# Kernel tuning notes

Measured on AMD Instinct MI355X. Metric: run time of the kernel, lower is better.

Reference implementation:

```python
import jax, jax.numpy as jnp
import numpy as np
import math

H, W, K = 512, 512, 256
EPS = 1e-6


def _make_grid(H, W):
    # Faithful to make_coord_grid: grid[a, b] = (xs[a], ys[b]) after the
    # torch meshgrid('xy') + permute(1,0,2) dance. With H == W this is (H, W, 2).
    xs = jnp.linspace(-1.0, 1.0, W)
    ys = jnp.linspace(-1.0, 1.0, H)
    X, Y = jnp.meshgrid(xs, ys, indexing='ij')  # (W, H)
    return jnp.stack([X, Y], axis=-1)  # (W, H, 2) == (H, W, 2) here


def setup_inputs() -> dict:
    key = jax.random.key(0)
    k_mu, k_theta, k_color = jax.random.split(key, 3)
    grid = _make_grid(H, W).astype(jnp.float32)
    mu = jax.random.uniform(k_mu, (K, 2), minval=-0.8, maxval=0.8, dtype=jnp.float32)
    log_scales = jnp.full((K, 2), math.log(0.3), dtype=jnp.float32)
    theta = jax.random.uniform(k_theta, (K,), minval=-math.pi, maxval=math.pi, dtype=jnp.float32)
    color_logits = 0.5 * jax.random.normal(k_color, (K, 3), dtype=jnp.float32)
    log_amp = jnp.full((K, 1), math.log(0.5), dtype=jnp.float32)
    return {
        'grid': grid,
        'mu': mu,
        'log_scales': log_scales,
        'theta': theta,
        'color_logits': color_logits,
        'log_amp': log_amp,
    }


def reference(grid, mu, log_scales, theta, color_logits, log_amp):
    scales = jnp.exp(log_scales)                      # (K, 2)
    sx, sy = scales[:, 0], scales[:, 1]
    # per-pixel, per-Gaussian offsets: (H, W, K)
    dx = grid[:, :, None, 0] - mu[None, None, :, 0]
    dy = grid[:, :, None, 1] - mu[None, None, :, 1]
    c, s = jnp.cos(theta), jnp.sin(theta)
    vx = dx * c + dy * s
    vy = -dx * s + dy * c
    q = vx * vx / (sx * sx + EPS) + vy * vy / (sy * sy + EPS)
    G = jnp.exp(-0.5 * q)                             # (H, W, K)
    amp = jax.nn.softplus(log_amp)[:, 0]              # (K,)
    weights = G * amp
    colors = jax.nn.sigmoid(color_logits)             # (K, 3)
    num = jnp.einsum('hwk,kc->hwc', weights, colors)  # (H, W, 3)
    den = jnp.sum(weights, axis=-1, keepdims=True)    # (H, W, 1)
    img = jnp.clip(num / (den + EPS), 0.0, 1.0)
    return img
```

## Files before the change

### kernel.cpp

```cpp
#include <hip/hip_runtime.h>
#include <hip/hip_bf16.h>
#include <math.h>

#define HH   512
#define WW   512
#define KG   256
#define EPSF 1e-6f
#define LOG2E 1.4426950408889634f

typedef short bf16x8 __attribute__((ext_vector_type(8)));
typedef float f32x4  __attribute__((ext_vector_type(4)));

union FragU { unsigned u[4]; bf16x8 v; };

__device__ __forceinline__ unsigned pkbf(float a, float b) {
    unsigned r;
    asm("v_cvt_pk_bf16_f32 %0, %1, %2" : "=v"(r) : "v"(a), "v"(b));
    return r;
}

#define SIDX(k) ((((k) & 7) << 5) + ((k) >> 3))

__global__ __launch_bounds__(512, 2) void gauss_render(
    const float* __restrict__ grid,
    const float* __restrict__ mu,
    const float* __restrict__ log_scales,
    const float* __restrict__ theta,
    const float* __restrict__ color_logits,
    const float* __restrict__ log_amp,
    float* __restrict__ out)
{
    __shared__ float4 sA[KG];
    __shared__ float4 sC[KG];
    __shared__ uint4  pkA4[8 * 17];
    __shared__ float  sY[WW];

    const int tid = threadIdx.x;
    const int col = blockIdx.x;

    const float2 p = reinterpret_cast<const float2*>(grid)[col * WW + tid];
    sY[tid] = p.y;
    const float X = p.x;

    if (tid < KG) {
        const int k = tid;
        const float mx  = mu[2 * k + 0];
        const float my  = mu[2 * k + 1];
        const float sx  = expf(log_scales[2 * k + 0]);
        const float sy  = expf(log_scales[2 * k + 1]);
        const float isx = 1.0f / (sx * sx + EPSF);
        const float isy = 1.0f / (sy * sy + EPSF);
        const float t   = theta[k];
        const float c   = cosf(t);
        const float s   = sinf(t);

        const float A = c * c * isx + s * s * isy;
        const float B = s * s * isx + c * c * isy;
        const float C = 2.0f * c * s * (isx - isy);

        const float la  = log_amp[k];
        const float amp = (la > 20.0f) ? la : log1pf(expf(la));
        const float lnA = logf(amp);

        const float ca = -0.5f * LOG2E * A;
        const float cb = -0.5f * LOG2E * B;
        const float cc = -0.5f * LOG2E * C;
        const float cd = LOG2E * (A * mx + 0.5f * C * my);
        const float ce = LOG2E * (B * my + 0.5f * C * mx);
        const float cf = LOG2E * (lnA - 0.5f * (A * mx * mx + B * my * my + C * mx * my));

        const float c0 = 1.0f / (1.0f + expf(-color_logits[3 * k + 0]));
        const float c1 = 1.0f / (1.0f + expf(-color_logits[3 * k + 1]));
        const float c2 = 1.0f / (1.0f + expf(-color_logits[3 * k + 2]));

        const float b1 = fmaf(cc, X, ce);
        const float b0 = fmaf(fmaf(ca, X, cd), X, cf);

        sA[SIDX(k)] = make_float4(b0, b1, cb, 0.0f);
        sC[k]       = make_float4(c0 - 0.5f, c1 - 0.5f, c2 - 0.5f, 1.0f);
    }
    __syncthreads();

    if (tid < 128) {
        const int m  = tid;
        const int kt = m >> 4, g = (m >> 2) & 3, i = m & 3;
        unsigned* pw = reinterpret_cast<unsigned*>(pkA4);
        #pragma unroll
        for (int ch = 0; ch < 4; ++ch) {
            const unsigned v = pkbf(((const float*)&sC[2 * m    ])[ch],
                                    ((const float*)&sC[2 * m + 1])[ch]);
            pw[(kt * 17 + ch * 4 + g) * 4 + i] = v;
        }
    }
    if (tid < 8) pkA4[tid * 17 + 16] = make_uint4(0u, 0u, 0u, 0u);
    __syncthreads();

    const int lane = tid & 63;
    const int wv   = tid >> 6;
    const int cidx = lane & 15;
    const int g    = lane >> 4;
    const int aOff = (cidx < 4) ? (cidx * 4 + g) : 16;

    float Yt[4];
    #pragma unroll
    for (int t = 0; t < 4; ++t)
        Yt[t] = sY[(wv * 4 + t) * 16 + cidx];

    f32x4 acc0 = {0.f,0.f,0.f,0.f}, acc1 = {0.f,0.f,0.f,0.f};
    f32x4 acc2 = {0.f,0.f,0.f,0.f}, acc3 = {0.f,0.f,0.f,0.f};

    #pragma unroll 1
    for (int kt = 0; kt < 8; ++kt) {
        const int bk = kt * 32 + g * 8;

        FragU af;
        {
            const uint4 av = pkA4[kt * 17 + aOff];
            af.u[0] = av.x; af.u[1] = av.y; af.u[2] = av.z; af.u[3] = av.w;
        }

        FragU b0f, b1f, b2f, b3f;
        #pragma unroll
        for (int i = 0; i < 4; ++i) {
            const int k0 = bk + 2 * i;
            const float4 q0 = sA[SIDX(k0)];
            const float4 q1 = sA[SIDX(k0 + 1)];

            {
                const float e0 = fmaf(fmaf(q0.z, Yt[0], q0.y), Yt[0], q0.x);
                const float e1 = fmaf(fmaf(q1.z, Yt[0], q1.y), Yt[0], q1.x);
                b0f.u[i] = pkbf(__builtin_amdgcn_exp2f(e0), __builtin_amdgcn_exp2f(e1));
            }
            {
                const float e0 = fmaf(fmaf(q0.z, Yt[1], q0.y), Yt[1], q0.x);
                const float e1 = fmaf(fmaf(q1.z, Yt[1], q1.y), Yt[1], q1.x);
                b1f.u[i] = pkbf(__builtin_amdgcn_exp2f(e0), __builtin_amdgcn_exp2f(e1));
            }
            {
                const float e0 = fmaf(fmaf(q0.z, Yt[2], q0.y), Yt[2], q0.x);
                const float e1 = fmaf(fmaf(q1.z, Yt[2], q1.y), Yt[2], q1.x);
                b2f.u[i] = pkbf(__builtin_amdgcn_exp2f(e0), __builtin_amdgcn_exp2f(e1));
            }
            {
                const float e0 = fmaf(fmaf(q0.z, Yt[3], q0.y), Yt[3], q0.x);
                const float e1 = fmaf(fmaf(q1.z, Yt[3], q1.y), Yt[3], q1.x);
                b3f.u[i] = pkbf(__builtin_amdgcn_exp2f(e0), __builtin_amdgcn_exp2f(e1));
            }
        }

        acc0 = __builtin_amdgcn_mfma_f32_16x16x32_bf16(af.v, b0f.v, acc0, 0, 0, 0);
        acc1 = __builtin_amdgcn_mfma_f32_16x16x32_bf16(af.v, b1f.v, acc1, 0, 0, 0);
        acc2 = __builtin_amdgcn_mfma_f32_16x16x32_bf16(af.v, b2f.v, acc2, 0, 0, 0);
        acc3 = __builtin_amdgcn_mfma_f32_16x16x32_bf16(af.v, b3f.v, acc3, 0, 0, 0);
    }

    if (lane < 16) {
        #pragma unroll
        for (int t = 0; t < 4; ++t) {
            const f32x4 acc = (t == 0) ? acc0 : (t == 1) ? acc1 : (t == 2) ? acc2 : acc3;
            const int pix = col * WW + (wv * 4 + t) * 16 + lane;
            const float inv = 1.0f / (acc[3] + EPSF);
            const float r   = fmaf(0.5f, acc[3], acc[0]) * inv;
            const float gch = fmaf(0.5f, acc[3], acc[1]) * inv;
            const float bch = fmaf(0.5f, acc[3], acc[2]) * inv;
            out[3 * pix + 0] = fminf(fmaxf(r,   0.0f), 1.0f);
            out[3 * pix + 1] = fminf(fmaxf(gch, 0.0f), 1.0f);
            out[3 * pix + 2] = fminf(fmaxf(bch, 0.0f), 1.0f);
        }
    }
}

extern "C" void kernel_launch(void* const* d_in, const int* in_sizes, int n_in,
                              void* d_out, int out_size, void* d_ws, size_t ws_size,
                              hipStream_t stream) {
    const float* grid         = (const float*)d_in[0];
    const float* mu           = (const float*)d_in[1];
    const float* log_scales   = (const float*)d_in[2];
    const float* theta        = (const float*)d_in[3];
    const float* color_logits = (const float*)d_in[4];
    const float* log_amp      = (const float*)d_in[5];
    float* out = (float*)d_out;

    const int threads = 512;
    const int blocks  = HH;
    hipLaunchKernelGGL(gauss_render, dim3(blocks), dim3(threads), 0, stream,
                       grid, mu, log_scales, theta, color_logits, log_amp, out);
}
```

Before: 17.34 us.

## Replace per-row exp2 with geometric recurrence across 4 grid rows

Instead of evaluating one exp2 for each of the four pixel rows a thread handles, each thread evaluates exp2 at the first row, then gets the next rows by multiplying with a ratio. The ratio itself is updated with a precomputed per-Gaussian constant stored in the spare sA slot. This follows from the quadratic exponent being evaluated on a uniformly spaced grid. It cuts transcendental work from 4 to 2 exp2 per Gaussian pair-element and relies on the grid spacing being exactly 32/511 in y. Chained multiplies can underflow or lose precision where the first row's weight is tiny.

```diff
diff --git a/kernel.cpp b/kernel.cpp
--- a/kernel.cpp
+++ b/kernel.cpp
@@ -7,6 +7,7 @@
 #define KG   256
 #define EPSF 1e-6f
 #define LOG2E 1.4426950408889634f
+#define DGRID (32.0f / 511.0f)
 
 typedef short bf16x8 __attribute__((ext_vector_type(8)));
 typedef float f32x4  __attribute__((ext_vector_type(4)));
@@ -75,8 +76,9 @@
 
         const float b1 = fmaf(cc, X, ce);
         const float b0 = fmaf(fmaf(ca, X, cd), X, cf);
+        const float cr = __builtin_amdgcn_exp2f(2.0f * cb * DGRID * DGRID);
 
-        sA[SIDX(k)] = make_float4(b0, b1, cb, 0.0f);
+        sA[SIDX(k)] = make_float4(b0, b1, cb, cr);
         sC[k]       = make_float4(c0 - 0.5f, c1 - 0.5f, c2 - 0.5f, 1.0f);
     }
     __syncthreads();
@@ -101,10 +103,8 @@
     const int g    = lane >> 4;
     const int aOff = (cidx < 4) ? (cidx * 4 + g) : 16;
 
-    float Yt[4];
-    #pragma unroll
-    for (int t = 0; t < 4; ++t)
-        Yt[t] = sY[(wv * 4 + t) * 16 + cidx];
+    const float Y0  = sY[wv * 64 + cidx];
+    const float Y2D = 2.0f * Y0 + DGRID;
 
     f32x4 acc0 = {0.f,0.f,0.f,0.f}, acc1 = {0.f,0.f,0.f,0.f};
     f32x4 acc2 = {0.f,0.f,0.f,0.f}, acc3 = {0.f,0.f,0.f,0.f};
@@ -126,26 +126,26 @@
             const float4 q0 = sA[SIDX(k0)];
             const float4 q1 = sA[SIDX(k0 + 1)];
 
-            {
-                const float e0 = fmaf(fmaf(q0.z, Yt[0], q0.y), Yt[0], q0.x);
-                const float e1 = fmaf(fmaf(q1.z, Yt[0], q1.y), Yt[0], q1.x);
-                b0f.u[i] = pkbf(__builtin_amdgcn_exp2f(e0), __builtin_amdgcn_exp2f(e1));
-            }
-            {
-                const float e0 = fmaf(fmaf(q0.z, Yt[1], q0.y), Yt[1], q0.x);
-                const float e1 = fmaf(fmaf(q1.z, Yt[1], q1.y), Yt[1], q1.x);
-                b1f.u[i] = pkbf(__builtin_amdgcn_exp2f(e0), __builtin_amdgcn_exp2f(e1));
-            }
-            {
-                const float e0 = fmaf(fmaf(q0.z, Yt[2], q0.y), Yt[2], q0.x);
-                const float e1 = fmaf(fmaf(q1.z, Yt[2], q1.y), Yt[2], q1.x);
-                b2f.u[i] = pkbf(__builtin_amdgcn_exp2f(e0), __builtin_amdgcn_exp2f(e1));
-            }
-            {
-                const float e0 = fmaf(fmaf(q0.z, Yt[3], q0.y), Yt[3], q0.x);
-                const float e1 = fmaf(fmaf(q1.z, Yt[3], q1.y), Yt[3], q1.x);
-                b3f.u[i] = pkbf(__builtin_amdgcn_exp2f(e0), __builtin_amdgcn_exp2f(e1));
-            }
+            const float e0a = fmaf(fmaf(q0.z, Y0, q0.y), Y0, q0.x);
+            const float dta = DGRID * fmaf(q0.z, Y2D, q0.y);
+            float       ra  = __builtin_amdgcn_exp2f(dta);
+            const float w0a = __builtin_amdgcn_exp2f(e0a);
+            const float w1a = w0a * ra;  ra *= q0.w;
+            const float w2a = w1a * ra;  ra *= q0.w;
+            const float w3a = w2a * ra;
+
+            const float e0b = fmaf(fmaf(q1.z, Y0, q1.y), Y0, q1.x);
+            const float dtb = DGRID * fmaf(q1.z, Y2D, q1.y);
+            float       rb  = __builtin_amdgcn_exp2f(dtb);
+            const float w0b = __builtin_amdgcn_exp2f(e0b);
+            const float w1b = w0b * rb;  rb *= q1.w;
+            const float w2b = w1b * rb;  rb *= q1.w;
+            const float w3b = w2b * rb;
+
+            b0f.u[i] = pkbf(w0a, w0b);
+            b1f.u[i] = pkbf(w1a, w1b);
+            b2f.u[i] = pkbf(w2a, w2b);
+            b3f.u[i] = pkbf(w3a, w3b);
         }
 
         acc0 = __builtin_amdgcn_mfma_f32_16x16x32_bf16(af.v, b0f.v, acc0, 0, 0, 0);
```

Result: faster. 15.50 us (median of 2 runs) (-10.6%).
